# Kernel optimization log

Hardware: AMD Instinct MI355X
Metric: run time of the kernel (lower is better)

The kernel has to match this reference:

```python
import jax, jax.numpy as jnp
import numpy as np

D_MODEL = 2048
NUM_HEADS = 16
D_KV = D_MODEL // NUM_HEADS
THETA = 10000.0
N_LORA = 4
RANK = 16
BATCH = 2
SEQ = 2048


def setup_inputs() -> dict:
    key = jax.random.key(0)
    ks = jax.random.split(key, 16)
    s = 0.02
    inp = {
        'x': jax.random.normal(ks[0], (BATCH, SEQ, D_MODEL), jnp.float32),
        'lora_start_indices': jnp.sort(jax.random.randint(ks[1], (N_LORA,), 0, BATCH)),
        'Wq': jax.random.normal(ks[2], (D_MODEL, D_MODEL), jnp.float32) * s,
        'Aq': jax.random.normal(ks[3], (N_LORA, RANK, D_MODEL), jnp.float32) * s,
        'Bq': jax.random.normal(ks[4], (N_LORA, D_MODEL, RANK), jnp.float32) * s,
        'Wk': jax.random.normal(ks[5], (D_MODEL, D_MODEL), jnp.float32) * s,
        'Ak': jax.random.normal(ks[6], (N_LORA, RANK, D_MODEL), jnp.float32) * s,
        'Bk': jax.random.normal(ks[7], (N_LORA, D_MODEL, RANK), jnp.float32) * s,
        'Wv': jax.random.normal(ks[8], (D_MODEL, D_MODEL), jnp.float32) * s,
        'Av': jax.random.normal(ks[9], (N_LORA, RANK, D_MODEL), jnp.float32) * s,
        'Bv': jax.random.normal(ks[10], (N_LORA, D_MODEL, RANK), jnp.float32) * s,
        'Wo': jax.random.normal(ks[11], (D_MODEL, D_MODEL), jnp.float32) * s,
        'Ao': jax.random.normal(ks[12], (N_LORA, RANK, D_MODEL), jnp.float32) * s,
        'Bo': jax.random.normal(ks[13], (N_LORA, D_MODEL, RANK), jnp.float32) * s,
    }
    return inp


def _adapter_ids(starts, batch):
    # each batch row b uses the adapter whose start index is the last one <= b
    ids = jnp.searchsorted(starts, jnp.arange(batch), side='right') - 1
    return jnp.clip(ids, 0, starts.shape[0] - 1)


def _multilora(x, ids, W, A, B):
    # x: [b, s, d_in]; W: [d_out, d_in]; A: [L, r, d_in]; B: [L, d_out, r]
    base = jnp.einsum('bsd,od->bso', x, W)
    Ai, Bi = A[ids], B[ids]                       # [b, r, d_in], [b, d_out, r]
    low = jnp.einsum('bsd,brd->bsr', x, Ai)
    return base + jnp.einsum('bsr,bor->bso', low, Bi)


def _rope(x):
    # x: [b, h, s, d]; interleaved pair rotation
    d = x.shape[-1]
    pos = jnp.arange(x.shape[-2], dtype=jnp.float32)
    inv_freq = THETA ** (-jnp.arange(0, d, 2, dtype=jnp.float32) / d)  # [d/2]
    ang = pos[:, None] * inv_freq[None, :]                              # [s, d/2]
    cos, sin = jnp.cos(ang), jnp.sin(ang)
    x1, x2 = x[..., 0::2], x[..., 1::2]
    o1 = x1 * cos - x2 * sin
    o2 = x1 * sin + x2 * cos
    return jnp.stack([o1, o2], axis=-1).reshape(x.shape)


def reference(x, lora_start_indices, Wq, Aq, Bq, Wk, Ak, Bk, Wv, Av, Bv, Wo, Ao, Bo):
    b, s, _ = x.shape
    ids = _adapter_ids(lora_start_indices, b)
    Q = _multilora(x, ids, Wq, Aq, Bq)
    K = _multilora(x, ids, Wk, Ak, Bk)
    V = _multilora(x, ids, Wv, Av, Bv)
    # [b, s, h*d] -> [b, h, s, d]
    split = lambda t: t.reshape(b, s, NUM_HEADS, D_KV).transpose(0, 2, 1, 3)
    Q, K, V = split(Q), split(K), split(V)
    Q, K = _rope(Q), _rope(K)
    scores = jnp.einsum('bhqd,bhkd->bhqk', Q, K) / jnp.sqrt(jnp.asarray(D_KV, x.dtype))
    causal = jnp.tril(jnp.ones((s, s), bool))
    scores = jnp.where(causal, scores, jnp.asarray(-jnp.inf, scores.dtype))
    attn = jax.nn.softmax(scores, axis=-1)
    out = jnp.einsum('bhqk,bhkd->bhqd', attn, V)
    out = out.transpose(0, 2, 1, 3).reshape(b, s, D_MODEL)
    return _multilora(out, ids, Wo, Ao, Bo)
```

## Files before the change

kernel.cpp:

```cpp
#include <hip/hip_runtime.h>

typedef unsigned short u16;
typedef unsigned int   u32;
typedef __bf16  bf16x8 __attribute__((ext_vector_type(8)));
typedef float   f32x4  __attribute__((ext_vector_type(4)));

#define D_MODEL 2048
#define SEQ     2048
#define NHEAD   16
#define DKV     128
#define RANK    16

__device__ __forceinline__ u16 f2b(float f) {
  union { float f; u32 i; } v; v.f = f;
  u32 i = v.i;
  return (u16)((i + 0x7FFFu + ((i >> 16) & 1u)) >> 16);
}
__device__ __forceinline__ u32 pack2(float lo, float hi) {
  return (u32)f2b(lo) | ((u32)f2b(hi) << 16);
}
__device__ __forceinline__ float b2f(u16 u) {
  union { u32 i; float f; } v; v.i = ((u32)u) << 16; return v.f;
}
__device__ __forceinline__ float dot2(u32 xa, u32 aa) {
  return b2f((u16)(xa & 0xFFFFu)) * b2f((u16)(aa & 0xFFFFu)) +
         b2f((u16)(xa >> 16))     * b2f((u16)(aa >> 16));
}
__device__ __forceinline__ int adapter_id(const int* starts, int b) {
  int cnt = 0;
#pragma unroll
  for (int i = 0; i < 4; ++i) cnt += (starts[i] <= b) ? 1 : 0;
  int id = cnt - 1;
  return id < 0 ? 0 : (id > 3 ? 3 : id);
}
__device__ __forceinline__ f32x4 mfma16(bf16x8 a, bf16x8 b, f32x4 c) {
  return __builtin_amdgcn_mfma_f32_16x16x32_bf16(a, b, c, 0, 0, 0);
}
__device__ __forceinline__ void gload16(const u16* g, u16* l) {
  __builtin_amdgcn_global_load_lds(
      (const __attribute__((address_space(1))) void*)g,
      (__attribute__((address_space(3))) void*)l, 16, 0, 0);
}

struct CvtArgs {
  const float* src[13];
  u32 base[14];
};
__global__ __launch_bounds__(256) void k_convert(CvtArgs a, u16* __restrict__ dst) {
  const u32 c = blockIdx.x * 256 + threadIdx.x;
  const u32 el0 = c * 8;
  if (el0 >= a.base[13]) return;
  int t = 0;
#pragma unroll
  for (int i = 1; i < 13; ++i) t += (el0 >= a.base[i]) ? 1 : 0;
  const float* s = a.src[t] + (el0 - a.base[t]);
  const float4 lo = *(const float4*)s;
  const float4 hi = *(const float4*)(s + 4);
  uint4 r;
  r.x = pack2(lo.x, lo.y); r.y = pack2(lo.z, lo.w);
  r.z = pack2(hi.x, hi.y); r.w = pack2(hi.z, hi.w);
  *(uint4*)(dst + el0) = r;
}

template <int TAG>
__global__ __launch_bounds__(256) void k_lowrank(
    const u16* __restrict__ X, const u16* __restrict__ A0,
    const u16* __restrict__ A1, const u16* __restrict__ A2,
    const int* __restrict__ starts, float* __restrict__ low, int nout)
{
  const int m = blockIdx.x;
  const int w = threadIdx.x >> 6, lane = threadIdx.x & 63;
  const int id = adapter_id(starts, m >> 11);
  const u16* Xr = X + (size_t)m * D_MODEL;
  for (int o = w; o < nout; o += 4) {
    const int p = o >> 4, r = o & 15;
    const u16* Ar = (p == 0 ? A0 : p == 1 ? A1 : A2) + (size_t)(id * 16 + r) * D_MODEL;
    float sum = 0.f;
#pragma unroll
    for (int c = 0; c < 4; ++c) {
      const int d = c * 512 + lane * 8;
      const uint4 xv = *(const uint4*)(Xr + d);
      const uint4 av = *(const uint4*)(Ar + d);
      sum += dot2(xv.x, av.x) + dot2(xv.y, av.y) + dot2(xv.z, av.z) + dot2(xv.w, av.w);
    }
#pragma unroll
    for (int off = 32; off >= 1; off >>= 1) sum += __shfl_xor(sum, off, 64);
    if (lane == 0) low[(size_t)m * nout + o] = sum;
  }
}

template <int QKV>
__global__ __launch_bounds__(256, 2) void k_gemm(
    const u16* __restrict__ X,
    const u16* __restrict__ W0, const u16* __restrict__ W1, const u16* __restrict__ W2,
    const u16* __restrict__ B0, const u16* __restrict__ B1, const u16* __restrict__ B2,
    const float* __restrict__ low, int ldlow,
    const int* __restrict__ starts,
    u16* __restrict__ D0, u16* __restrict__ D1, u16* __restrict__ D2,
    float* __restrict__ Df)
{
  __shared__ __attribute__((aligned(16))) u16 At[128 * 64];
  __shared__ __attribute__((aligned(16))) u16 Bt[128 * 64];
  const int tid = threadIdx.x;
  const int w = tid >> 6, lane = tid & 63, quad = lane >> 4, l16 = lane & 15;
  const int wr = w >> 1, wc = w & 1;

  const int nwg = gridDim.x * gridDim.y * gridDim.z;
  const int cpx = nwg >> 3;
  const int lin = blockIdx.x + gridDim.x * (blockIdx.y + gridDim.y * blockIdx.z);
  const int nl  = (lin & 7) * cpx + (lin >> 3);
  const int n0 = (nl & 15) * 128, m0 = ((nl >> 4) & 31) * 128, z = nl >> 9;

  const u16* W  = (z == 0) ? W0 : (z == 1) ? W1 : W2;
  const u16* Bm = (z == 0) ? B0 : (z == 1) ? B1 : B2;
  u16*       D  = (z == 0) ? D0 : (z == 1) ? D1 : D2;
  const int loff = QKV ? z * RANK : 0;
  const int id = adapter_id(starts, m0 >> 11);

  const f32x4 zero4 = {0.f, 0.f, 0.f, 0.f};
  f32x4 acc[4][4];
#pragma unroll
  for (int i = 0; i < 4; ++i)
#pragma unroll
    for (int j = 0; j < 4; ++j) acc[i][j] = zero4;

  const int srow_l = lane >> 3;
  const int sgran  = (lane & 7) ^ srow_l;
  const u16* gA = X + (size_t)(m0 + w * 32 + srow_l) * D_MODEL + sgran * 8;
  const u16* gB = W + (size_t)(n0 + w * 32 + srow_l) * D_MODEL + sgran * 8;
  u16* lA = At + (w * 32) * 64;
  u16* lB = Bt + (w * 32) * 64;

  for (int kt = 0; kt < D_MODEL / 64; ++kt) {
    const int kb = kt * 64;
#pragma unroll
    for (int c = 0; c < 4; ++c)
      gload16(gA + (size_t)(c * 8) * D_MODEL + kb, lA + c * 8 * 64);
#pragma unroll
    for (int c = 0; c < 4; ++c)
      gload16(gB + (size_t)(c * 8) * D_MODEL + kb, lB + c * 8 * 64);
    __syncthreads();
#pragma unroll
    for (int kk = 0; kk < 2; ++kk) {
      bf16x8 af[4], bfr[4];
#pragma unroll
      for (int i = 0; i < 4; ++i) {
        const int row = wr * 64 + i * 16 + l16;
        af[i] = *(const bf16x8*)&At[row * 64 + (((kk * 4 + quad) ^ (l16 & 7)) * 8)];
      }
#pragma unroll
      for (int j = 0; j < 4; ++j) {
        const int row = wc * 64 + j * 16 + l16;
        bfr[j] = *(const bf16x8*)&Bt[row * 64 + (((kk * 4 + quad) ^ (l16 & 7)) * 8)];
      }
#pragma unroll
      for (int i = 0; i < 4; ++i)
#pragma unroll
        for (int j = 0; j < 4; ++j)
          acc[i][j] = mfma16(af[i], bfr[j], acc[i][j]);
    }
    __syncthreads();
  }

  for (int e = tid; e < 4096; e += 256) {
    const int rr = e >> 5, kk = e & 31;
    u16 av = 0, bv = 0;
    if (kk < RANK) {
      av = f2b(low[(size_t)(m0 + rr) * ldlow + loff + kk]);
      bv = Bm[((size_t)id * D_MODEL + n0 + rr) * RANK + kk];
    }
    At[rr * 64 + (kk ^ ((rr & 7) << 3))] = av;
    Bt[rr * 64 + (kk ^ ((rr & 7) << 3))] = bv;
  }
  __syncthreads();
  {
    bf16x8 af[4], bfr[4];
#pragma unroll
    for (int i = 0; i < 4; ++i) {
      const int row = wr * 64 + i * 16 + l16;
      af[i] = *(const bf16x8*)&At[row * 64 + ((quad ^ (l16 & 7)) * 8)];
    }
#pragma unroll
    for (int j = 0; j < 4; ++j) {
      const int row = wc * 64 + j * 16 + l16;
      bfr[j] = *(const bf16x8*)&Bt[row * 64 + ((quad ^ (l16 & 7)) * 8)];
    }
#pragma unroll
    for (int i = 0; i < 4; ++i)
#pragma unroll
      for (int j = 0; j < 4; ++j)
        acc[i][j] = mfma16(af[i], bfr[j], acc[i][j]);
  }

  if (QKV) {
    const float scale = (z == 0) ? 0.08838834764831845f : 1.0f;
    const int ropez = (z <= 1);
#pragma unroll
    for (int i = 0; i < 4; ++i) {
      const int mrow = m0 + wr * 64 + i * 16 + quad * 4;
#pragma unroll
      for (int j = 0; j < 4; ++j) {
        const int col = n0 + wc * 64 + j * 16 + l16;
        const int hh = col >> 7, jj = col & (DKV - 1);
        const float invf = exp2f(-0.20762050593046f * (float)(jj >> 1));
#pragma unroll
        for (int r = 0; r < 4; ++r) {
          const int m = mrow + r;
          const int bb = m >> 11, srw = m & (SEQ - 1);
          float v = acc[i][j][r] * scale;
          if (ropez) {
            float sn, cs;
            __sincosf((float)srw * invf, &sn, &cs);
            const float part = __shfl_xor(v, 1, 64);
            v = (jj & 1) ? (part * sn + v * cs) : (v * cs - part * sn);
          }
          D[(((size_t)(bb * NHEAD + hh)) * SEQ + srw) * DKV + jj] = f2b(v);
        }
      }
    }
  } else {
#pragma unroll
    for (int i = 0; i < 4; ++i) {
      const int mrow = m0 + wr * 64 + i * 16 + quad * 4;
#pragma unroll
      for (int j = 0; j < 4; ++j) {
        const int col = n0 + wc * 64 + j * 16 + l16;
#pragma unroll
        for (int r = 0; r < 4; ++r)
          Df[(size_t)(mrow + r) * D_MODEL + col] = acc[i][j][r];
      }
    }
  }
}

#define M0 8.0f
__global__ __launch_bounds__(256, 2) void k_flash(
    const u16* __restrict__ Q, const u16* __restrict__ K,
    const u16* __restrict__ V, u16* __restrict__ O,
    u16* __restrict__ Opart, float* __restrict__ lpart)
{
  __shared__ __attribute__((aligned(16))) u16 Kl[64 * 128];
  __shared__ __attribute__((aligned(16))) u16 VT[DKV * 64];
  __shared__ __attribute__((aligned(16))) u16 Pl[4 * 32 * 64];
  const int tid = threadIdx.x;
  const int w = tid >> 6, lane = tid & 63, quad = lane >> 4, l16 = lane & 15;
  const int lin = blockIdx.x + 16 * blockIdx.y;
  const int nlb = (lin & 7) * 64 + (lin >> 3);
  const int pj = nlb & 15, bh = nlb >> 4;
  const int pid = pj >> 1, j = pj & 1;
  const size_t base = (size_t)bh * SEQ * DKV;
  const u16* Qb = Q + base;
  const u16* Kb = K + base;
  const u16* Vb = V + base;
  const int b = bh >> 4, h = bh & 15;
  u16* Plw = &Pl[w * 2048];
  const f32x4 zero4 = {0.f, 0.f, 0.f, 0.f};

  const int qtB = 15 - pid;
  const int A_steps = (j == 0) ? (2 * pid + 2) : 0;
  const int kt0 = (j == 0) ? 0 : (15 - 2 * pid);

  int qt = (j == 0) ? pid : qtB;
  int q0 = qt * 128;

  bf16x8 qa[2][4];
#pragma unroll
  for (int h2 = 0; h2 < 2; ++h2)
#pragma unroll
    for (int kc = 0; kc < 4; ++kc)
      qa[h2][kc] = *(const bf16x8*)(Qb + (size_t)(q0 + w * 32 + h2 * 16 + l16) * DKV + kc * 32 + quad * 8);

  f32x4 oacc[2][8];
#pragma unroll
  for (int h2 = 0; h2 < 2; ++h2)
#pragma unroll
    for (int nn = 0; nn < 8; ++nn) oacc[h2][nn] = zero4;
  float lr[2][4] = {{0.f,0.f,0.f,0.f},{0.f,0.f,0.f,0.f}};

  const int krr = tid >> 4;
  const int kc8 = (tid & 15) * 8;
  const int kswz = (krr & 7) * 8;
  const int vrp = tid & 31;
  const int vcg = tid >> 5;

  uint4 pk[4], pva[2], pvb[2];
  {
    const size_t ko = (size_t)((j == 0) ? 0 : kt0) * 64 * DKV;
#pragma unroll
    for (int it = 0; it < 4; ++it)
      pk[it] = *(const uint4*)(Kb + ko + (size_t)(krr + it * 16) * DKV + kc8);
#pragma unroll
    for (int it = 0; it < 2; ++it) {
      pva[it] = *(const uint4*)(Vb + ko + (size_t)(2 * vrp)     * DKV + (vcg + it * 8) * 8);
      pvb[it] = *(const uint4*)(Vb + ko + (size_t)(2 * vrp + 1) * DKV + (vcg + it * 8) * 8);
    }
  }

  for (int s = 0; s < 17; ++s) {
    if (j == 0 && s == A_steps) {
      float inv[2][4];
#pragma unroll
      for (int h2 = 0; h2 < 2; ++h2)
#pragma unroll
        for (int rg = 0; rg < 4; ++rg) {
          float t = lr[h2][rg];
#pragma unroll
          for (int off = 8; off >= 1; off >>= 1) t += __shfl_xor(t, off, 64);
          inv[h2][rg] = 1.f / t;
          lr[h2][rg] = 0.f;
        }
#pragma unroll
      for (int h2 = 0; h2 < 2; ++h2)
#pragma unroll
        for (int nn = 0; nn < 8; ++nn) {
          const int col = h * DKV + nn * 16 + l16;
#pragma unroll
          for (int rg = 0; rg < 4; ++rg) {
            const int row = q0 + w * 32 + h2 * 16 + quad * 4 + rg;
            O[((size_t)b * SEQ + row) * D_MODEL + col] = f2b(oacc[h2][nn][rg] * inv[h2][rg]);
          }
#pragma unroll
          for (int e = 0; e < 4; ++e) oacc[h2][nn][e] = 0.f;
        }
      qt = qtB; q0 = qt * 128;
#pragma unroll
      for (int h2 = 0; h2 < 2; ++h2)
#pragma unroll
        for (int kc = 0; kc < 4; ++kc)
          qa[h2][kc] = *(const bf16x8*)(Qb + (size_t)(q0 + w * 32 + h2 * 16 + l16) * DKV + kc * 32 + quad * 8);
    }
    const int kt = (j == 0) ? ((s < A_steps) ? s : s - A_steps) : kt0 + s;

    __syncthreads();
#pragma unroll
    for (int it = 0; it < 4; ++it)
      *(uint4*)(&Kl[(krr + it * 16) * 128 + (kc8 ^ kswz)]) = pk[it];
#pragma unroll
    for (int it = 0; it < 2; ++it) {
      const int c0 = (vcg + it * 8) * 8;
      const uint4 a = pva[it], c = pvb[it];
#define VTW(k, val) *(u32*)&VT[(c0 + (k)) * 64 + ((2 * vrp) ^ (((c0 + (k)) & 7) * 8))] = (val)
      VTW(0, (a.x & 0xFFFFu) | (c.x << 16));
      VTW(1, (a.x >> 16)     | (c.x & 0xFFFF0000u));
      VTW(2, (a.y & 0xFFFFu) | (c.y << 16));
      VTW(3, (a.y >> 16)     | (c.y & 0xFFFF0000u));
      VTW(4, (a.z & 0xFFFFu) | (c.z << 16));
      VTW(5, (a.z >> 16)     | (c.z & 0xFFFF0000u));
      VTW(6, (a.w & 0xFFFFu) | (c.w << 16));
      VTW(7, (a.w >> 16)     | (c.w & 0xFFFF0000u));
#undef VTW
    }
    __syncthreads();

    if (s + 1 < 17) {
      const int sn = s + 1;
      const int ktn = (j == 0) ? ((sn < A_steps) ? sn : sn - A_steps) : kt0 + sn;
      const size_t ko = (size_t)ktn * 64 * DKV;
#pragma unroll
      for (int it = 0; it < 4; ++it)
        pk[it] = *(const uint4*)(Kb + ko + (size_t)(krr + it * 16) * DKV + kc8);
#pragma unroll
      for (int it = 0; it < 2; ++it) {
        pva[it] = *(const uint4*)(Vb + ko + (size_t)(2 * vrp)     * DKV + (vcg + it * 8) * 8);
        pvb[it] = *(const uint4*)(Vb + ko + (size_t)(2 * vrp + 1) * DKV + (vcg + it * 8) * 8);
      }
    }

    f32x4 sacc[2][4];
#pragma unroll
    for (int h2 = 0; h2 < 2; ++h2)
#pragma unroll
      for (int jc = 0; jc < 4; ++jc) sacc[h2][jc] = zero4;
#pragma unroll
    for (int kc = 0; kc < 4; ++kc)
#pragma unroll
      for (int jc = 0; jc < 4; ++jc) {
        const bf16x8 kb = *(const bf16x8*)&Kl[(jc * 16 + l16) * 128 + ((kc * 32 + quad * 8) ^ ((l16 & 7) * 8))];
        sacc[0][jc] = mfma16(qa[0][kc], kb, sacc[0][jc]);
        sacc[1][jc] = mfma16(qa[1][kc], kb, sacc[1][jc]);
      }

    const int diag = (kt >= 2 * qt);
#pragma unroll
    for (int h2 = 0; h2 < 2; ++h2)
#pragma unroll
      for (int rg = 0; rg < 4; ++rg) {
        const int qq = q0 + w * 32 + h2 * 16 + quad * 4 + rg;
        const int row_p = h2 * 16 + quad * 4 + rg;
        float psum = 0.f;
#pragma unroll
        for (int jc = 0; jc < 4; ++jc) {
          const int kk = kt * 64 + jc * 16 + l16;
          float p = __expf(sacc[h2][jc][rg] - M0);
          if (diag && kk > qq) p = 0.f;
          psum += p;
          const int col = jc * 16 + l16;
          Plw[row_p * 64 + (col ^ ((row_p & 7) * 8))] = f2b(p);
        }
        lr[h2][rg] += psum;
      }

#pragma unroll
    for (int kc = 0; kc < 2; ++kc) {
      const int pswz = (kc * 32 + quad * 8) ^ ((l16 & 7) * 8);
      const bf16x8 pa0 = *(const bf16x8*)&Plw[(     l16) * 64 + pswz];
      const bf16x8 pa1 = *(const bf16x8*)&Plw[(16 + l16) * 64 + pswz];
#pragma unroll
      for (int nn = 0; nn < 8; ++nn) {
        const bf16x8 vb = *(const bf16x8*)&VT[(nn * 16 + l16) * 64 + pswz];
        oacc[0][nn] = mfma16(pa0, vb, oacc[0][nn]);
        oacc[1][nn] = mfma16(pa1, vb, oacc[1][nn]);
      }
    }
  }

  const int slot = (bh * 8 + (7 - pid)) * 2 + j;
#pragma unroll
  for (int h2 = 0; h2 < 2; ++h2)
#pragma unroll
    for (int rg = 0; rg < 4; ++rg) {
#pragma unroll
      for (int off = 8; off >= 1; off >>= 1) lr[h2][rg] += __shfl_xor(lr[h2][rg], off, 64);
    }
#pragma unroll
  for (int h2 = 0; h2 < 2; ++h2)
#pragma unroll
    for (int nn = 0; nn < 8; ++nn) {
#pragma unroll
      for (int rg = 0; rg < 4; ++rg) {
        const int row = w * 32 + h2 * 16 + quad * 4 + rg;
        Opart[(size_t)slot * 16384 + row * 128 + nn * 16 + l16] = f2b(oacc[h2][nn][rg]);
      }
    }
  if (l16 == 0) {
#pragma unroll
    for (int h2 = 0; h2 < 2; ++h2)
#pragma unroll
      for (int rg = 0; rg < 4; ++rg)
        lpart[slot * 128 + w * 32 + h2 * 16 + quad * 4 + rg] = lr[h2][rg];
  }
}

__global__ __launch_bounds__(256) void k_merge(
    const u16* __restrict__ Opart, const float* __restrict__ lpart,
    u16* __restrict__ O)
{
  const u32 t = blockIdx.x * 256 + threadIdx.x;
  const u32 u   = t & 63;
  const u32 row = (t >> 6) & 127;
  const u32 t8  = (t >> 13) & 7;
  const u32 bh  = t >> 16;
  const u32 slot0 = (bh * 8 + t8) * 2;
  const u32 o0 = slot0 * 8192u + row * 64u + u;
  const u32 a = ((const u32*)Opart)[o0];
  const u32 c = ((const u32*)Opart)[o0 + 8192];
  const float inv = 1.f / (lpart[slot0 * 128 + row] + lpart[(slot0 + 1) * 128 + row]);
  const float r0 = (b2f((u16)(a & 0xFFFFu)) + b2f((u16)(c & 0xFFFFu))) * inv;
  const float r1 = (b2f((u16)(a >> 16))     + b2f((u16)(c >> 16)))     * inv;
  const u32 bb = bh >> 4, h = bh & 15;
  const u32 s = (t8 + 8) * 128 + row;
  ((u32*)O)[(size_t)(bb * SEQ + s) * (D_MODEL / 2) + h * 64 + u] = pack2(r0, r1);
}

extern "C" void kernel_launch(void* const* d_in, const int* in_sizes, int n_in,
                              void* d_out, int out_size, void* d_ws, size_t ws_size,
                              hipStream_t stream) {
  (void)in_sizes; (void)n_in; (void)out_size; (void)ws_size;
  const int* starts = (const int*)d_in[1];

  static const u32 XB = 0;
  static const u32 WQ = 8388608, WK = 12582912, WV = 16777216, WO = 20971520;
  static const u32 AQ = 25165824, AK = 25296896, AV = 25427968, AO = 25559040;
  static const u32 BQ = 25690112, BK = 25821184, BV = 25952256, BO = 26083328;
  static const u32 TOT = 26214400;

  u16* wsb = (u16*)d_ws;
  char* ws = (char*)d_ws;
  float* low_qkv = (float*)(ws + 52428800);
  float* low_o   = (float*)(ws + 53215232);
  u16*   Qb      = (u16*)(ws + 53477376);
  u16*   Kb      = (u16*)(ws + 70254592);
  u16*   Vb      = (u16*)(ws + 87031808);
  u16*   attn    = wsb + XB;
  u16*   Opart   = (u16*)d_out;
  float* lpart   = (float*)((char*)d_out + 16777216);

  CvtArgs ca;
  ca.src[0]  = (const float*)d_in[0];
  ca.src[1]  = (const float*)d_in[2];
  ca.src[2]  = (const float*)d_in[5];
  ca.src[3]  = (const float*)d_in[8];
  ca.src[4]  = (const float*)d_in[11];
  ca.src[5]  = (const float*)d_in[3];
  ca.src[6]  = (const float*)d_in[6];
  ca.src[7]  = (const float*)d_in[9];
  ca.src[8]  = (const float*)d_in[12];
  ca.src[9]  = (const float*)d_in[4];
  ca.src[10] = (const float*)d_in[7];
  ca.src[11] = (const float*)d_in[10];
  ca.src[12] = (const float*)d_in[13];
  const u32 bases[14] = {XB, WQ, WK, WV, WO, AQ, AK, AV, AO, BQ, BK, BV, BO, TOT};
  for (int i = 0; i < 14; ++i) ca.base[i] = bases[i];

  k_convert<<<dim3(TOT / 8 / 256), 256, 0, stream>>>(ca, wsb);

  k_lowrank<0><<<dim3(4096), 256, 0, stream>>>(wsb + XB, wsb + AQ, wsb + AK, wsb + AV,
                                               starts, low_qkv, 48);
  k_gemm<1><<<dim3(16, 32, 3), 256, 0, stream>>>(
      wsb + XB, wsb + WQ, wsb + WK, wsb + WV, wsb + BQ, wsb + BK, wsb + BV,
      low_qkv, 48, starts, Qb, Kb, Vb, (float*)nullptr);
  k_flash<<<dim3(16, 32), 256, 0, stream>>>(Qb, Kb, Vb, attn, Opart, lpart);
  k_merge<<<dim3(8192), 256, 0, stream>>>(Opart, lpart, attn);
  k_lowrank<1><<<dim3(4096), 256, 0, stream>>>(attn, wsb + AO, wsb + AO, wsb + AO,
                                               starts, low_o, 16);
  k_gemm<0><<<dim3(16, 32, 1), 256, 0, stream>>>(
      attn, wsb + WO, wsb + WO, wsb + WO, wsb + BO, wsb + BO, wsb + BO,
      low_o, 16, starts, (u16*)nullptr, (u16*)nullptr, (u16*)nullptr,
      (float*)d_out);
}
```

Measured before the change: 462.9 us.

## Fuse low-rank QKV into convert kernel and merge split-KV inside flash

Extra blocks are appended to the convert kernel to compute the QKV LoRA low-rank projections directly from fp32 inputs, removing a separate launch. The split-KV merge kernel is eliminated: each flash block increments an atomic counter and the second-arriving block of a pair merges the partial outputs. This cuts launch overhead and a separate pass over partials, at the cost of atomics, threadfences, and a serialized merge tail on some flash blocks.

```diff
diff --git a/kernel.cpp b/kernel.cpp
--- a/kernel.cpp
+++ b/kernel.cpp
@@ -46,8 +46,41 @@
   const float* src[13];
   u32 base[14];
 };
-__global__ __launch_bounds__(256) void k_convert(CvtArgs a, u16* __restrict__ dst) {
-  const u32 c = blockIdx.x * 256 + threadIdx.x;
+__global__ __launch_bounds__(256) void k_front(
+    CvtArgs a, u16* __restrict__ dst,
+    const float* __restrict__ xf,
+    const float* __restrict__ Aqf, const float* __restrict__ Akf,
+    const float* __restrict__ Avf,
+    const int* __restrict__ starts, float* __restrict__ low,
+    u32* __restrict__ cnt)
+{
+  const u32 blk = blockIdx.x;
+  const int tid = threadIdx.x;
+  if (blk >= 12800) {
+    const int m = (int)blk - 12800;
+    if (blk == 12800) cnt[tid] = 0;
+    const int w = tid >> 6, lane = tid & 63;
+    const int id = adapter_id(starts, m >> 11);
+    const float* Xr = xf + (size_t)m * D_MODEL;
+    for (int o = w; o < 48; o += 4) {
+      const int p = o >> 4, r = o & 15;
+      const float* Ar = (p == 0 ? Aqf : p == 1 ? Akf : Avf) +
+                        (size_t)(id * 16 + r) * D_MODEL;
+      float sum = 0.f;
+#pragma unroll
+      for (int c = 0; c < 8; ++c) {
+        const int d = c * 256 + lane * 4;
+        const float4 xv = *(const float4*)(Xr + d);
+        const float4 av = *(const float4*)(Ar + d);
+        sum += xv.x * av.x + xv.y * av.y + xv.z * av.z + xv.w * av.w;
+      }
+#pragma unroll
+      for (int off = 32; off >= 1; off >>= 1) sum += __shfl_xor(sum, off, 64);
+      if (lane == 0) low[(size_t)m * 48 + o] = sum;
+    }
+    return;
+  }
+  const u32 c = blk * 256 + tid;
   const u32 el0 = c * 8;
   if (el0 >= a.base[13]) return;
   int t = 0;
@@ -237,11 +270,13 @@
 __global__ __launch_bounds__(256, 2) void k_flash(
     const u16* __restrict__ Q, const u16* __restrict__ K,
     const u16* __restrict__ V, u16* __restrict__ O,
-    u16* __restrict__ Opart, float* __restrict__ lpart)
+    u16* __restrict__ Opart, float* __restrict__ lpart,
+    u32* __restrict__ cnt)
 {
   __shared__ __attribute__((aligned(16))) u16 Kl[64 * 128];
   __shared__ __attribute__((aligned(16))) u16 VT[DKV * 64];
   __shared__ __attribute__((aligned(16))) u16 Pl[4 * 32 * 64];
+  __shared__ int s_old;
   const int tid = threadIdx.x;
   const int w = tid >> 6, lane = tid & 63, quad = lane >> 4, l16 = lane & 15;
   const int lin = blockIdx.x + 16 * blockIdx.y;
@@ -439,27 +474,29 @@
       for (int rg = 0; rg < 4; ++rg)
         lpart[slot * 128 + w * 32 + h2 * 16 + quad * 4 + rg] = lr[h2][rg];
   }
-}
-
-__global__ __launch_bounds__(256) void k_merge(
-    const u16* __restrict__ Opart, const float* __restrict__ lpart,
-    u16* __restrict__ O)
-{
-  const u32 t = blockIdx.x * 256 + threadIdx.x;
-  const u32 u   = t & 63;
-  const u32 row = (t >> 6) & 127;
-  const u32 t8  = (t >> 13) & 7;
-  const u32 bh  = t >> 16;
-  const u32 slot0 = (bh * 8 + t8) * 2;
-  const u32 o0 = slot0 * 8192u + row * 64u + u;
-  const u32 a = ((const u32*)Opart)[o0];
-  const u32 c = ((const u32*)Opart)[o0 + 8192];
-  const float inv = 1.f / (lpart[slot0 * 128 + row] + lpart[(slot0 + 1) * 128 + row]);
-  const float r0 = (b2f((u16)(a & 0xFFFFu)) + b2f((u16)(c & 0xFFFFu))) * inv;
-  const float r1 = (b2f((u16)(a >> 16))     + b2f((u16)(c >> 16)))     * inv;
-  const u32 bb = bh >> 4, h = bh & 15;
-  const u32 s = (t8 + 8) * 128 + row;
-  ((u32*)O)[(size_t)(bb * SEQ + s) * (D_MODEL / 2) + h * 64 + u] = pack2(r0, r1);
+
+  __threadfence();
+  if (tid == 0) s_old = (int)atomicAdd(&cnt[slot >> 1], 1u);
+  __syncthreads();
+  if (s_old == 1) {
+    __threadfence();
+    const u32 g   = (u32)(slot >> 1);
+    const u32 t8  = g & 7;
+    const u32 bhg = g >> 3;
+    const u32 bbg = bhg >> 4, hg = bhg & 15;
+    const u32 base0 = 2u * g * 8192u;
+    for (int it = 0; it < 32; ++it) {
+      const u32 e = (u32)it * 256u + (u32)tid;
+      const u32 row = e >> 6, u = e & 63;
+      const u32 a = ((const u32*)Opart)[base0 + row * 64u + u];
+      const u32 c = ((const u32*)Opart)[base0 + 8192u + row * 64u + u];
+      const float inv = 1.f / (lpart[2u * g * 128u + row] + lpart[(2u * g + 1u) * 128u + row]);
+      const float r0 = (b2f((u16)(a & 0xFFFFu)) + b2f((u16)(c & 0xFFFFu))) * inv;
+      const float r1 = (b2f((u16)(a >> 16))     + b2f((u16)(c >> 16)))     * inv;
+      const u32 srow = (t8 + 8) * 128 + row;
+      ((u32*)O)[(size_t)(bbg * SEQ + srow) * (D_MODEL / 2) + hg * 64 + u] = pack2(r0, r1);
+    }
+  }
 }
 
 extern "C" void kernel_launch(void* const* d_in, const int* in_sizes, int n_in,
@@ -484,6 +521,7 @@
   u16*   attn    = wsb + XB;
   u16*   Opart   = (u16*)d_out;
   float* lpart   = (float*)((char*)d_out + 16777216);
+  u32*   cnt     = (u32*)(ws + 103809024);
 
   CvtArgs ca;
   ca.src[0]  = (const float*)d_in[0];
@@ -502,15 +540,14 @@
   const u32 bases[14] = {XB, WQ, WK, WV, WO, AQ, AK, AV, AO, BQ, BK, BV, BO, TOT};
   for (int i = 0; i < 14; ++i) ca.base[i] = bases[i];
 
-  k_convert<<<dim3(TOT / 8 / 256), 256, 0, stream>>>(ca, wsb);
-
-  k_lowrank<0><<<dim3(4096), 256, 0, stream>>>(wsb + XB, wsb + AQ, wsb + AK, wsb + AV,
-                                               starts, low_qkv, 48);
+  k_front<<<dim3(16896), 256, 0, stream>>>(
+      ca, wsb, (const float*)d_in[0], (const float*)d_in[3],
+      (const float*)d_in[6], (const float*)d_in[9], starts, low_qkv, cnt);
+
   k_gemm<1><<<dim3(16, 32, 3), 256, 0, stream>>>(
       wsb + XB, wsb + WQ, wsb + WK, wsb + WV, wsb + BQ, wsb + BK, wsb + BV,
       low_qkv, 48, starts, Qb, Kb, Vb, (float*)nullptr);
-  k_flash<<<dim3(16, 32), 256, 0, stream>>>(Qb, Kb, Vb, attn, Opart, lpart);
-  k_merge<<<dim3(8192), 256, 0, stream>>>(Opart, lpart, attn);
+  k_flash<<<dim3(16, 32), 256, 0, stream>>>(Qb, Kb, Vb, attn, Opart, lpart, cnt);
   k_lowrank<1><<<dim3(4096), 256, 0, stream>>>(attn, wsb + AO, wsb + AO, wsb + AO,
                                                starts, low_o, 16);
   k_gemm<0><<<dim3(16, 32, 1), 256, 0, stream>>>(
```

New measurement: 574.4 us. +24.1%, slower.
